# Performance work log

Hardware: AMD Instinct MI355X
Metric: run time of the kernel (lower is better)

## Reference

```python
import jax, jax.numpy as jnp
import numpy as np

N = 10000      # nodes
E = 320000     # edges
H = 128        # hidden_features
GF = 12        # graph-level features
L = 6          # gnn layers
EPS = 1e-5


def _glorot(key, shape):
    fan_in = shape[0]
    return (jax.random.normal(key, shape, jnp.float32) / np.sqrt(fan_in)).astype(jnp.float32)


def periodic_difference(x_i, x_j, domain):
    diff = x_i - x_j
    # (1 - 2*(x_i < x_j)) * domain  ==  +domain if x_i >= x_j else -domain
    shift = jnp.where(x_i < x_j, -domain, domain)
    diff_shifted = diff - shift
    return jnp.where(jnp.abs(diff) < jnp.abs(diff_shifted), diff, diff_shifted)


def _mlp2_relu(x, W1, b1, W2, b2):
    # Linear -> ReLU -> Linear -> ReLU
    return jax.nn.relu(jax.nn.relu(x @ W1 + b1) @ W2 + b2)


def setup_inputs() -> dict:
    key = jax.random.key(0)
    ks = jax.random.split(key, 32)
    inp = {
        "v": jax.random.normal(ks[0], (N, 6), jnp.float32),
        "pos": jax.random.uniform(ks[1], (N, 3), jnp.float32),
        "r": jax.random.uniform(ks[2], (N, 1), jnp.float32),
        "domain": jnp.ones((3,), jnp.float32),
        "t": jax.random.uniform(ks[3], (1,), jnp.float32),
        "x_global": jax.random.normal(ks[4], (4,), jnp.float32),
        "domain_next": jnp.ones((3,), jnp.float32),
        "t_next": jax.random.uniform(ks[5], (1,), jnp.float32),
        "edge_index": jax.random.randint(ks[6], (2, E), 0, N, jnp.int32),
        "batch": jnp.zeros((N,), jnp.int32),
    }
    # embedding MLP: 19 -> H -> H
    inp["emb_W1"] = _glorot(ks[7], (19, H)); inp["emb_b1"] = jnp.zeros((H,), jnp.float32)
    inp["emb_W2"] = _glorot(ks[8], (H, H)); inp["emb_b2"] = jnp.zeros((H,), jnp.float32)
    # per-layer message net: 157 -> H -> H ; update net: 268 -> H -> H
    msg_in = H + GF + 3 + 2 * (6 + 1)   # 157
    upd_in = H + H + GF                 # 268
    inp["msg_W1"] = jnp.stack([_glorot(jax.random.fold_in(ks[9], i), (msg_in, H)) for i in range(L)])
    inp["msg_b1"] = jnp.zeros((L, H), jnp.float32)
    inp["msg_W2"] = jnp.stack([_glorot(jax.random.fold_in(ks[10], i), (H, H)) for i in range(L)])
    inp["msg_b2"] = jnp.zeros((L, H), jnp.float32)
    inp["upd_W1"] = jnp.stack([_glorot(jax.random.fold_in(ks[11], i), (upd_in, H)) for i in range(L)])
    inp["upd_b1"] = jnp.zeros((L, H), jnp.float32)
    inp["upd_W2"] = jnp.stack([_glorot(jax.random.fold_in(ks[12], i), (H, H)) for i in range(L)])
    inp["upd_b2"] = jnp.zeros((L, H), jnp.float32)
    # output MLP: H -> H -> 9 ; macro MLP: H -> H -> 3
    inp["out_W1"] = _glorot(ks[13], (H, H)); inp["out_b1"] = jnp.zeros((H,), jnp.float32)
    inp["out_W2"] = _glorot(ks[14], (H, 9)); inp["out_b2"] = jnp.zeros((9,), jnp.float32)
    inp["mac_W1"] = _glorot(ks[15], (H, H)); inp["mac_b1"] = jnp.zeros((H,), jnp.float32)
    inp["mac_W2"] = _glorot(ks[16], (H, 3)); inp["mac_b2"] = jnp.zeros((3,), jnp.float32)
    return inp


def reference(v, pos, r, domain, t, x_global, domain_next, t_next, edge_index, batch,
              emb_W1, emb_b1, emb_W2, emb_b2,
              msg_W1, msg_b1, msg_W2, msg_b2,
              upd_W1, upd_b1, upd_W2, upd_b2,
              out_W1, out_b1, out_W2, out_b2,
              mac_W1, mac_b1, mac_W2, mac_b2):
    n = v.shape[0]
    gf = jnp.concatenate([domain, t, x_global, domain_next, t_next])          # [12]
    gf_n = jnp.broadcast_to(gf, (n, GF))
    node_features = jnp.concatenate([pos, v], axis=1)                         # [N, 9]

    # embedding (positions excluded)
    h = _mlp2_relu(jnp.concatenate([r, v, gf_n], axis=1), emb_W1, emb_b1, emb_W2, emb_b2)

    src, dst = edge_index[0], edge_index[1]   # j = source, i = target (PyG default)
    gf_e = jnp.broadcast_to(gf, (src.shape[0], GF))
    counts = jax.ops.segment_sum(jnp.ones(src.shape, h.dtype), dst, num_segments=N)
    inv_counts = (1.0 / jnp.maximum(counts, 1.0))[:, None]

    pos_diff = periodic_difference(pos[dst], pos[src], domain)                # [E, 3]
    v_i, v_j, r_i, r_j = v[dst], v[src], r[dst], r[src]

    for l in range(L):
        h_i, h_j = h[dst], h[src]
        msg_in = jnp.concatenate([h_i - h_j, v_i, v_j, r_i, r_j, pos_diff, gf_e], axis=1)
        m = _mlp2_relu(msg_in, msg_W1[l], msg_b1[l], msg_W2[l], msg_b2[l])    # [E, H]
        agg = jax.ops.segment_sum(m, dst, num_segments=N) * inv_counts        # scatter-mean
        upd_in = jnp.concatenate([h, agg, gf_n], axis=1)
        u = _mlp2_relu(upd_in, upd_W1[l], upd_b1[l], upd_W2[l], upd_b2[l])
        h = u + h                                                              # residual (in==out)
        # InstanceNorm over each graph (single graph here), biased variance
        mu = h.mean(axis=0, keepdims=True)
        var = h.var(axis=0, keepdims=True)
        h = (h - mu) / jnp.sqrt(var + EPS)

    prediction = jax.nn.relu(h @ out_W1 + out_b1) @ out_W2 + out_b2 + node_features
    pred_x = jnp.remainder(prediction[:, :3], domain_next)
    pred_v = prediction[:, 3:]
    h_mean = h.mean(axis=0)                                                    # global mean pool, 1 graph
    pred_macro = jax.nn.relu(h_mean @ mac_W1 + mac_b1) @ mac_W2 + mac_b2
    return pred_x, pred_v, pred_macro
```

## Files before the change

kernel.cpp:

```cpp
#include <hip/hip_runtime.h>
#include <hip/hip_bf16.h>

#define NN 10000
#define NE 320000
#define HD 128
#define NL 6
#define EPSV 1e-5f

typedef _Float16 half8  __attribute__((ext_vector_type(8)));
typedef _Float16 half4v __attribute__((ext_vector_type(4)));
typedef float    f32x4  __attribute__((ext_vector_type(4)));

__device__ __forceinline__ float relu_(float x){ return fmaxf(x, 0.0f); }


__global__ void k_degree(const int* __restrict__ dst, int* __restrict__ counts){
  int e = blockIdx.x*256 + threadIdx.x;
  if (e < NE) atomicAdd(&counts[dst[e]], 1);
}

__global__ void k_scan(const int* __restrict__ counts, int* __restrict__ offs, float* __restrict__ invc){
  __shared__ int lds[1024];
  __shared__ int base_s;
  int tid = threadIdx.x;
  if (tid==0) base_s = 0;
  __syncthreads();
  for (int start=0; start<NN; start+=1024){
    int i = start+tid;
    int vv = (i<NN)? counts[i] : 0;
    lds[tid]=vv; __syncthreads();
    for (int off=1; off<1024; off<<=1){
      int t = (tid>=off)? lds[tid-off] : 0;
      __syncthreads();
      lds[tid] += t;
      __syncthreads();
    }
    int incl = lds[tid];
    if (i<NN){
      offs[i] = base_s + incl - vv;
      invc[i] = 1.0f / fmaxf((float)vv, 1.0f);
    }
    __syncthreads();
    if (tid==1023) base_s += lds[1023];
    __syncthreads();
  }
  if (tid==0) offs[NN] = base_s;
}

__global__ void k_place(const int* __restrict__ src, const int* __restrict__ dst,
                        const int* __restrict__ offs, int* __restrict__ cursor, int* __restrict__ csr){
  int e = blockIdx.x*256 + threadIdx.x;
  if (e < NE){
    int d = dst[e];
    int p = atomicAdd(&cursor[d], 1);
    csr[offs[d]+p] = src[e];
  }
}


__global__ void k_biasfold(const float* __restrict__ dom, const float* __restrict__ tt,
                           const float* __restrict__ xg, const float* __restrict__ domn,
                           const float* __restrict__ tn,
                           const float* __restrict__ embW1, const float* __restrict__ embB1,
                           const float* __restrict__ msgW1, const float* __restrict__ msgB1,
                           const float* __restrict__ updW1, const float* __restrict__ updB1,
                           float* __restrict__ b1eff, float* __restrict__ mu, float* __restrict__ rstd){
  float gf[12];
  gf[0]=dom[0]; gf[1]=dom[1]; gf[2]=dom[2]; gf[3]=tt[0];
  gf[4]=xg[0]; gf[5]=xg[1]; gf[6]=xg[2]; gf[7]=xg[3];
  gf[8]=domn[0]; gf[9]=domn[1]; gf[10]=domn[2]; gf[11]=tn[0];
  int b = blockIdx.x, t = threadIdx.x;
  if (b==0){
    float s = embB1[t];
    #pragma unroll
    for (int k=0;k<12;++k) s += gf[k]*embW1[(7+k)*HD + t];
    b1eff[t] = s;
  } else if (b<=6){
    int l=b-1;
    float s = msgB1[l*HD+t];
    #pragma unroll
    for (int k=0;k<12;++k) s += gf[k]*msgW1[((size_t)l*157 + 145+k)*HD + t];
    b1eff[(1+l)*HD + t] = s;
  } else if (b<=12){
    int l=b-7;
    float s = updB1[l*HD+t];
    #pragma unroll
    for (int k=0;k<12;++k) s += gf[k]*updW1[((size_t)l*268 + 256+k)*HD + t];
    b1eff[(7+l)*HD + t] = s;
  } else {
    mu[t] = 0.f;
    rstd[t] = 1.f;
  }
}


__global__ void k_embed(const float* __restrict__ r, const float* __restrict__ v,
                        const float* __restrict__ W1, const float* __restrict__ b1e,
                        const float* __restrict__ W2, const float* __restrict__ b2,
                        float* __restrict__ hb){
  __shared__ alignas(16) float a1s[4][HD];
  int tid=threadIdx.x, wid=tid>>6, lane=tid&63;
  int gw = blockIdx.x*4 + wid;
  int f0=lane, f1=lane+64;
  float* a1 = a1s[wid];
  float b1f0=b1e[f0], b1f1=b1e[f1], b2f0=b2[f0], b2f1=b2[f1];
  for (int n=gw*4; n<gw*4+4; ++n){
    float in7[7];
    in7[0]=r[n];
    #pragma unroll
    for (int k=0;k<6;++k) in7[1+k]=v[n*6+k];
    float z0=b1f0, z1=b1f1;
    #pragma unroll
    for (int k=0;k<7;++k){ z0 += in7[k]*W1[k*HD+f0]; z1 += in7[k]*W1[k*HD+f1]; }
    a1[f0]=relu_(z0); a1[f1]=relu_(z1);
    float h0=b2f0, h1=b2f1;
    for (int k=0;k<HD;++k){ float a=a1[k]; h0+=a*W2[k*HD+f0]; h1+=a*W2[k*HD+f1]; }
    hb[n*HD+f0]=relu_(h0); hb[n*HD+f1]=relu_(h1);
  }
}


__global__ __launch_bounds__(512,1) void k_hW(
    const float* __restrict__ hb, const float* __restrict__ mu, const float* __restrict__ rstd,
    const float* __restrict__ v, const float* __restrict__ r,
    const float* __restrict__ W, const float* __restrict__ b1e,
    float* __restrict__ P, float* __restrict__ Q){
  __shared__ alignas(16) _Float16 Xhi[16*136];
  __shared__ alignas(16) _Float16 Xlo[16*136];
  int tid = threadIdx.x;
  int n0 = blockIdx.x*16;
  if (tid < 256){
    int node = tid>>4, chunk = tid&15;
    int n = n0 + node;
    int f = chunk*8;
    half8 xh, xl;
    #pragma unroll
    for (int j=0;j<8;++j){
      float x = (hb[(size_t)n*HD + f+j] - mu[f+j]) * rstd[f+j];
      _Float16 h = (_Float16)x;
      xh[j] = h; xl[j] = (_Float16)(x - (float)h);
    }
    *(half8*)&Xhi[node*136 + f] = xh;
    *(half8*)&Xlo[node*136 + f] = xl;
  }
  int wid = tid>>6, lane = tid&63, g = lane>>4, c = lane&15;
  int col = 16*wid + c;
  half8 bh[4], bl[4];
  #pragma unroll
  for (int ks=0; ks<4; ++ks){
    half8 fh, fl;
    #pragma unroll
    for (int j=0;j<8;++j){
      float w = W[(size_t)(ks*32 + g*8 + j)*HD + col];
      _Float16 h = (_Float16)w;
      fh[j]=h; fl[j]=(_Float16)(w - (float)h);
    }
    bh[ks]=fh; bl[ks]=fl;
  }
  float wvi[6], wvj[6];
  #pragma unroll
  for (int x=0;x<6;++x){
    wvi[x]=W[(size_t)(128+x)*HD+col];
    wvj[x]=W[(size_t)(134+x)*HD+col];
  }
  float wri=W[(size_t)140*HD+col], wrj=W[(size_t)141*HD+col];
  float b1c=b1e[col];
  f32x4 zero4 = {0.f,0.f,0.f,0.f};
  __syncthreads();
  f32x4 d = zero4;
  #pragma unroll
  for (int ks=0; ks<4; ++ks){
    half8 ah = *(const half8*)&Xhi[c*136 + ks*32 + g*8];
    half8 al = *(const half8*)&Xlo[c*136 + ks*32 + g*8];
    d = __builtin_amdgcn_mfma_f32_16x16x32_f16(ah, bh[ks], d, 0,0,0);
    d = __builtin_amdgcn_mfma_f32_16x16x32_f16(al, bh[ks], d, 0,0,0);
    d = __builtin_amdgcn_mfma_f32_16x16x32_f16(ah, bl[ks], d, 0,0,0);
  }
  #pragma unroll
  for (int jj=0;jj<4;++jj){
    int n = n0 + g*4 + jj;
    float m = d[jj];
    float p = m + b1c, q = -m;
    #pragma unroll
    for (int x=0;x<6;++x){
      float vx = v[n*6+x];
      p += vx*wvi[x]; q += vx*wvj[x];
    }
    float rn = r[n];
    p += rn*wri; q += rn*wrj;
    P[(size_t)n*HD+col]=p;
    Q[(size_t)n*HD+col]=q;
  }
}


__global__ __launch_bounds__(256,2) void k_edge(
    const float* __restrict__ P, const float* __restrict__ Q,
    const float* __restrict__ pos, const float* __restrict__ dom,
    const int* __restrict__ offs, const int* __restrict__ csr,
    const float* __restrict__ Wpd, const float* __restrict__ W2, const float* __restrict__ b2,
    const float* __restrict__ invc, float* __restrict__ agg,
    float* __restrict__ zsum, float* __restrict__ zsumsq){
  __shared__ alignas(16) _Float16 w1pd[128*40];
  __shared__ alignas(16) _Float16 a1hi[16*136];
  __shared__ alignas(16) _Float16 a1lo[16*136];
  int tid = threadIdx.x;
  if (blockIdx.x==0 && tid<HD){ zsum[tid]=0.f; zsumsq[tid]=0.f; }
  if (tid < 128){
    int f = tid;
    #pragma unroll
    for (int k=0;k<32;++k) w1pd[f*40+k] = (_Float16)0.f;
    #pragma unroll
    for (int x=0;x<3;++x){
      float w = Wpd[x*HD + f];
      _Float16 h = (_Float16)w;
      w1pd[f*40 + x]     = h;
      w1pd[f*40 + 3 + x] = h;
      w1pd[f*40 + 6 + x] = (_Float16)(w - (float)h);
    }
  }
  int wid = tid>>6, lane = tid&63, g = lane>>4, c = lane&15;
  int t0 = 2*wid, t1 = 2*wid+1;
  half8 w2h[4][2], w2l[4][2];
  #pragma unroll
  for (int ks=0; ks<4; ++ks){
    #pragma unroll
    for (int tt=0; tt<2; ++tt){
      int col = 16*(2*wid+tt) + c;
      half8 fh, fl;
      #pragma unroll
      for (int j=0;j<8;++j){
        float w = W2[(ks*32 + g*8 + j)*HD + col];
        _Float16 h = (_Float16)w;
        fh[j] = h;
        fl[j] = (_Float16)(w - (float)h);
      }
      w2h[ks][tt] = fh;
      w2l[ks][tt] = fl;
    }
  }
  float b2v0 = b2[16*t0 + c], b2v1 = b2[16*t1 + c];
  float dm0=dom[0], dm1=dom[1], dm2=dom[2];
  f32x4 zero4 = {0.f,0.f,0.f,0.f};
  __syncthreads();
  int n0 = blockIdx.x*4;
  for (int n = n0; n < n0+4; ++n){
    f32x4 pv0 = *(const f32x4*)(P + (size_t)n*HD + 16*t0 + 4*g);
    f32x4 pv1 = *(const f32x4*)(P + (size_t)n*HD + 16*t1 + 4*g);
    float pn0=pos[n*3+0], pn1=pos[n*3+1], pn2=pos[n*3+2];
    float acc0=0.f, acc1=0.f;
    int ib=offs[n], ie=offs[n+1];
    for (int base=ib; base<ie; base+=16){
      int nb = ie - base; if (nb>16) nb = 16;
      int sA = csr[base + ((c<nb)? c : nb-1)];
      float q0=pos[sA*3+0], q1=pos[sA*3+1], q2=pos[sA*3+2];
      float pd0,pd1,pd2;
      { float diff,sh,ds;
        diff=pn0-q0; sh=(pn0<q0)?-dm0:dm0; ds=diff-sh; pd0=(fabsf(diff)<fabsf(ds))?diff:ds;
        diff=pn1-q1; sh=(pn1<q1)?-dm1:dm1; ds=diff-sh; pd1=(fabsf(diff)<fabsf(ds))?diff:ds;
        diff=pn2-q2; sh=(pn2<q2)?-dm2:dm2; ds=diff-sh; pd2=(fabsf(diff)<fabsf(ds))?diff:ds;
      }
      _Float16 p0h = (_Float16)pd0, p1h = (_Float16)pd1, p2h = (_Float16)pd2;
      _Float16 p0l = (_Float16)(pd0 - (float)p0h);
      _Float16 p1l = (_Float16)(pd1 - (float)p1h);
      _Float16 p2l = (_Float16)(pd2 - (float)p2h);
      half8 pdf;
      #pragma unroll
      for (int j=0;j<8;++j) pdf[j]=(_Float16)0.f;
      if (g==0){ pdf[0]=p0h; pdf[1]=p1h; pdf[2]=p2h; pdf[3]=p0l; pdf[4]=p1l; pdf[5]=p2l; pdf[6]=p0h; pdf[7]=p1h; }
      else if (g==1){ pdf[0]=p2h; }
      half8 w1f0 = *(const half8*)&w1pd[(16*t0 + c)*40 + g*8];
      half8 w1f1 = *(const half8*)&w1pd[(16*t1 + c)*40 + g*8];
      f32x4 d0 = __builtin_amdgcn_mfma_f32_16x16x32_f16(w1f0, pdf, zero4, 0,0,0);
      f32x4 d1 = __builtin_amdgcn_mfma_f32_16x16x32_f16(w1f1, pdf, zero4, 0,0,0);
      const float* Qs = Q + (size_t)sA*HD;
      f32x4 qv0 = *(const f32x4*)(Qs + 16*t0 + 4*g);
      f32x4 qv1 = *(const f32x4*)(Qs + 16*t1 + 4*g);
      half4v h0, l0, h1, l1;
      #pragma unroll
      for (int j=0;j<4;++j){
        float a = fmaxf(d0[j] + pv0[j] + qv0[j], 0.f);
        _Float16 hh = (_Float16)a;
        h0[j] = hh; l0[j] = (_Float16)(a - (float)hh);
        float b = fmaxf(d1[j] + pv1[j] + qv1[j], 0.f);
        _Float16 hb2 = (_Float16)b;
        h1[j] = hb2; l1[j] = (_Float16)(b - (float)hb2);
      }
      *(half4v*)&a1hi[c*136 + 16*t0 + 4*g] = h0;
      *(half4v*)&a1lo[c*136 + 16*t0 + 4*g] = l0;
      *(half4v*)&a1hi[c*136 + 16*t1 + 4*g] = h1;
      *(half4v*)&a1lo[c*136 + 16*t1 + 4*g] = l1;
      __syncthreads();
      f32x4 m0 = zero4, m1 = zero4;
      #pragma unroll
      for (int ks=0; ks<4; ++ks){
        half8 ah = *(const half8*)&a1hi[c*136 + ks*32 + g*8];
        half8 al = *(const half8*)&a1lo[c*136 + ks*32 + g*8];
        m0 = __builtin_amdgcn_mfma_f32_16x16x32_f16(ah, w2h[ks][0], m0, 0,0,0);
        m0 = __builtin_amdgcn_mfma_f32_16x16x32_f16(al, w2h[ks][0], m0, 0,0,0);
        m0 = __builtin_amdgcn_mfma_f32_16x16x32_f16(ah, w2l[ks][0], m0, 0,0,0);
        m1 = __builtin_amdgcn_mfma_f32_16x16x32_f16(ah, w2h[ks][1], m1, 0,0,0);
        m1 = __builtin_amdgcn_mfma_f32_16x16x32_f16(al, w2h[ks][1], m1, 0,0,0);
        m1 = __builtin_amdgcn_mfma_f32_16x16x32_f16(ah, w2l[ks][1], m1, 0,0,0);
      }
      if (nb == 16){
        acc0 += fmaxf(m0[0]+b2v0,0.f)+fmaxf(m0[1]+b2v0,0.f)+fmaxf(m0[2]+b2v0,0.f)+fmaxf(m0[3]+b2v0,0.f);
        acc1 += fmaxf(m1[0]+b2v1,0.f)+fmaxf(m1[1]+b2v1,0.f)+fmaxf(m1[2]+b2v1,0.f)+fmaxf(m1[3]+b2v1,0.f);
      } else {
        #pragma unroll
        for (int j=0;j<4;++j){
          if (4*g+j < nb){
            acc0 += fmaxf(m0[j]+b2v0, 0.f);
            acc1 += fmaxf(m1[j]+b2v1, 0.f);
          }
        }
      }
      __syncthreads();
    }
    acc0 += __shfl_xor(acc0, 16); acc0 += __shfl_xor(acc0, 32);
    acc1 += __shfl_xor(acc1, 16); acc1 += __shfl_xor(acc1, 32);
    if (g==0){
      float ic = invc[n];
      agg[n*HD + 16*t0 + c] = acc0*ic;
      agg[n*HD + 16*t1 + c] = acc1*ic;
    }
  }
}


__global__ __launch_bounds__(512,1) void k_upd(
    float* __restrict__ hb, const float* __restrict__ mu, const float* __restrict__ rstd,
    const float* __restrict__ agg,
    const float* __restrict__ U1, const float* __restrict__ b1e,
    const float* __restrict__ U2, const float* __restrict__ bs2,
    float* __restrict__ sum, float* __restrict__ sumsq){
  __shared__ alignas(16) _Float16 Xhi[16*264];
  __shared__ alignas(16) _Float16 Xlo[16*264];
  __shared__ alignas(16) _Float16 Ahi[16*136];
  __shared__ alignas(16) _Float16 Alo[16*136];
  int tid = threadIdx.x;
  int n0 = blockIdx.x*16;
  {
    int node = tid>>5, chunk = tid&31;
    int n = n0 + node;
    int f = chunk*8;
    half8 xh, xl;
    if (f < 128){
      #pragma unroll
      for (int j=0;j<8;++j){
        float x = (hb[(size_t)n*HD + f+j] - mu[f+j]) * rstd[f+j];
        _Float16 h = (_Float16)x;
        xh[j] = h; xl[j] = (_Float16)(x - (float)h);
      }
    } else {
      #pragma unroll
      for (int j=0;j<8;++j){
        float x = agg[(size_t)n*HD + (f-128)+j];
        _Float16 h = (_Float16)x;
        xh[j] = h; xl[j] = (_Float16)(x - (float)h);
      }
    }
    *(half8*)&Xhi[node*264 + f] = xh;
    *(half8*)&Xlo[node*264 + f] = xl;
  }
  int wid = tid>>6, lane = tid&63, g = lane>>4, c = lane&15;
  int col = 16*wid + c;
  half8 b1h[8], b1l[8], b2h[4], b2l[4];
  #pragma unroll
  for (int ks=0; ks<8; ++ks){
    half8 fh, fl;
    #pragma unroll
    for (int j=0;j<8;++j){
      float w = U1[(size_t)(ks*32 + g*8 + j)*HD + col];
      _Float16 h = (_Float16)w;
      fh[j]=h; fl[j]=(_Float16)(w - (float)h);
    }
    b1h[ks]=fh; b1l[ks]=fl;
  }
  #pragma unroll
  for (int ks=0; ks<4; ++ks){
    half8 fh, fl;
    #pragma unroll
    for (int j=0;j<8;++j){
      float w = U2[(size_t)(ks*32 + g*8 + j)*HD + col];
      _Float16 h = (_Float16)w;
      fh[j]=h; fl[j]=(_Float16)(w - (float)h);
    }
    b2h[ks]=fh; b2l[ks]=fl;
  }
  f32x4 zero4 = {0.f,0.f,0.f,0.f};
  __syncthreads();
  f32x4 d = zero4;
  #pragma unroll
  for (int ks=0; ks<8; ++ks){
    half8 ah = *(const half8*)&Xhi[c*264 + ks*32 + g*8];
    half8 al = *(const half8*)&Xlo[c*264 + ks*32 + g*8];
    d = __builtin_amdgcn_mfma_f32_16x16x32_f16(ah, b1h[ks], d, 0,0,0);
    d = __builtin_amdgcn_mfma_f32_16x16x32_f16(al, b1h[ks], d, 0,0,0);
    d = __builtin_amdgcn_mfma_f32_16x16x32_f16(ah, b1l[ks], d, 0,0,0);
  }
  {
    float bb = b1e[col];
    #pragma unroll
    for (int jj=0;jj<4;++jj){
      float a = fmaxf(d[jj] + bb, 0.f);
      _Float16 h = (_Float16)a;
      Ahi[(g*4+jj)*136 + col] = h;
      Alo[(g*4+jj)*136 + col] = (_Float16)(a - (float)h);
    }
  }
  __syncthreads();
  f32x4 u = zero4;
  #pragma unroll
  for (int ks=0; ks<4; ++ks){
    half8 ah = *(const half8*)&Ahi[c*136 + ks*32 + g*8];
    half8 al = *(const half8*)&Alo[c*136 + ks*32 + g*8];
    u = __builtin_amdgcn_mfma_f32_16x16x32_f16(ah, b2h[ks], u, 0,0,0);
    u = __builtin_amdgcn_mfma_f32_16x16x32_f16(al, b2h[ks], u, 0,0,0);
    u = __builtin_amdgcn_mfma_f32_16x16x32_f16(ah, b2l[ks], u, 0,0,0);
  }
  float bc = bs2[col];
  float mc = mu[col], rc = rstd[col];
  float s=0.f, q=0.f;
  #pragma unroll
  for (int jj=0;jj<4;++jj){
    int n = n0 + g*4 + jj;
    float hn = (hb[(size_t)n*HD + col] - mc)*rc;
    float b0 = hn + fmaxf(u[jj] + bc, 0.f);
    hb[(size_t)n*HD + col] = b0;
    s += b0; q += b0*b0;
  }
  s += __shfl_xor(s,16); s += __shfl_xor(s,32);
  q += __shfl_xor(q,16); q += __shfl_xor(q,32);
  if (g==0){
    atomicAdd(&sum[col], s);
    atomicAdd(&sumsq[col], q);
  }
}

__global__ void k_normfin(const float* __restrict__ sum, const float* __restrict__ sumsq,
                          float* __restrict__ mu, float* __restrict__ rstd){
  int t=threadIdx.x;
  float m = sum[t]*(1.0f/NN);
  float var = sumsq[t]*(1.0f/NN) - m*m;
  mu[t]=m;
  rstd[t]=rsqrtf(fmaxf(var,0.0f)+EPSV);
}


__global__ void k_out(const float* __restrict__ hb, const float* __restrict__ mu, const float* __restrict__ rstd,
                      const float* __restrict__ pos, const float* __restrict__ v,
                      const float* __restrict__ W1, const float* __restrict__ b1,
                      const float* __restrict__ W2, const float* __restrict__ b2,
                      const float* __restrict__ domn, float* __restrict__ out){
  __shared__ alignas(16) float hs[4][HD*4];
  __shared__ alignas(16) float a1s[4][HD*4];
  int tid=threadIdx.x, wid=tid>>6, lane=tid&63;
  int gw=blockIdx.x*4+wid;
  int f0=lane, f1=lane+64;
  float* h4=hs[wid];
  float* a1p=a1s[wid];
  int n0=gw*4;
  float mu0=mu[f0], mu1=mu[f1], rs0=rstd[f0], rs1=rstd[f1];
  float4 hv0,hv1;
  hv0.x=(hb[(n0+0)*HD+f0]-mu0)*rs0; hv0.y=(hb[(n0+1)*HD+f0]-mu0)*rs0;
  hv0.z=(hb[(n0+2)*HD+f0]-mu0)*rs0; hv0.w=(hb[(n0+3)*HD+f0]-mu0)*rs0;
  hv1.x=(hb[(n0+0)*HD+f1]-mu1)*rs1; hv1.y=(hb[(n0+1)*HD+f1]-mu1)*rs1;
  hv1.z=(hb[(n0+2)*HD+f1]-mu1)*rs1; hv1.w=(hb[(n0+3)*HD+f1]-mu1)*rs1;
  *(float4*)&h4[f0*4]=hv0; *(float4*)&h4[f1*4]=hv1;
  float b1f0=b1[f0], b1f1=b1[f1];
  float zf0[4]={b1f0,b1f0,b1f0,b1f0}, zf1[4]={b1f1,b1f1,b1f1,b1f1};
  for (int k=0;k<HD;++k){
    float4 a = *(const float4*)&h4[k*4];
    float w0=W1[k*HD+f0], w1=W1[k*HD+f1];
    zf0[0]+=a.x*w0; zf1[0]+=a.x*w1;
    zf0[1]+=a.y*w0; zf1[1]+=a.y*w1;
    zf0[2]+=a.z*w0; zf1[2]+=a.z*w1;
    zf0[3]+=a.w*w0; zf1[3]+=a.w*w1;
  }
  *(float4*)&a1p[f0*4] = make_float4(relu_(zf0[0]),relu_(zf0[1]),relu_(zf0[2]),relu_(zf0[3]));
  *(float4*)&a1p[f1*4] = make_float4(relu_(zf1[0]),relu_(zf1[1]),relu_(zf1[2]),relu_(zf1[3]));
  if (lane < 36){
    int e = lane/9, j = lane - e*9;
    int n = n0+e;
    float p = b2[j];
    for (int k=0;k<HD;++k) p += a1p[k*4+e]*W2[k*9+j];
    if (j<3){
      p += pos[n*3+j];
      float d = domn[j];
      p = p - floorf(p/d)*d;
      out[n*3+j] = p;
    } else {
      p += v[n*6 + (j-3)];
      out[3*NN + n*6 + (j-3)] = p;
    }
  }
}

__global__ void k_macro(const float* __restrict__ sum, const float* __restrict__ mu, const float* __restrict__ rstd,
                        const float* __restrict__ W1, const float* __restrict__ b1,
                        const float* __restrict__ W2, const float* __restrict__ b2,
                        float* __restrict__ out){
  __shared__ float hm[HD];
  __shared__ float as[HD];
  int t=threadIdx.x;
  hm[t] = (sum[t]*(1.0f/NN) - mu[t])*rstd[t];
  __syncthreads();
  float z=b1[t];
  for (int k=0;k<HD;++k) z += hm[k]*W1[k*HD+t];
  as[t]=relu_(z);
  __syncthreads();
  if (t<3){
    float p=b2[t];
    for (int k=0;k<HD;++k) p += as[k]*W2[k*3+t];
    out[9*NN+t]=p;
  }
}


extern "C" void kernel_launch(void* const* d_in, const int* in_sizes, int n_in,
                              void* d_out, int out_size, void* d_ws, size_t ws_size,
                              hipStream_t stream) {
  const float* v    = (const float*)d_in[0];
  const float* pos  = (const float*)d_in[1];
  const float* r    = (const float*)d_in[2];
  const float* dom  = (const float*)d_in[3];
  const float* tt   = (const float*)d_in[4];
  const float* xg   = (const float*)d_in[5];
  const float* domn = (const float*)d_in[6];
  const float* tn   = (const float*)d_in[7];
  const int*   eidx = (const int*)d_in[8];
  const float* embW1 = (const float*)d_in[10];
  const float* embB1 = (const float*)d_in[11];
  const float* embW2 = (const float*)d_in[12];
  const float* embB2 = (const float*)d_in[13];
  const float* msgW1 = (const float*)d_in[14];
  const float* msgB1 = (const float*)d_in[15];
  const float* msgW2 = (const float*)d_in[16];
  const float* msgB2 = (const float*)d_in[17];
  const float* updW1 = (const float*)d_in[18];
  const float* updB1 = (const float*)d_in[19];
  const float* updW2 = (const float*)d_in[20];
  const float* updB2 = (const float*)d_in[21];
  const float* outW1 = (const float*)d_in[22];
  const float* outB1 = (const float*)d_in[23];
  const float* outW2 = (const float*)d_in[24];
  const float* outB2 = (const float*)d_in[25];
  const float* macW1 = (const float*)d_in[26];
  const float* macB1 = (const float*)d_in[27];
  const float* macW2 = (const float*)d_in[28];
  const float* macB2 = (const float*)d_in[29];
  float* out = (float*)d_out;
  float* ws  = (float*)d_ws;

  float* hb    = ws;
  float* P     = ws + 1280000;
  float* Q     = ws + 2560000;
  float* agg   = ws + 3840000;
  float* invc  = ws + 5120000;
  float* b1eff = ws + 5130000;
  float* sum   = ws + 5131664;
  float* sumsq = ws + 5131792;
  float* mu    = ws + 5131920;
  float* rstd  = ws + 5132048;
  int* counts  = (int*)(ws + 5132304);
  int* offs    = counts + NN;
  int* cursor  = offs + NN + 1;
  int* csr     = cursor + NN;

  const int* srcA = eidx;
  const int* dstA = eidx + NE;

  hipMemsetAsync(counts, 0, NN*sizeof(int), stream);
  hipMemsetAsync(cursor, 0, NN*sizeof(int), stream);

  k_degree<<<(NE+255)/256, 256, 0, stream>>>(dstA, counts);
  k_scan<<<1, 1024, 0, stream>>>(counts, offs, invc);
  k_place<<<(NE+255)/256, 256, 0, stream>>>(srcA, dstA, offs, cursor, csr);
  k_biasfold<<<14, 128, 0, stream>>>(dom, tt, xg, domn, tn, embW1, embB1, msgW1, msgB1, updW1, updB1,
                                     b1eff, mu, rstd);
  k_embed<<<625, 256, 0, stream>>>(r, v, embW1, b1eff, embW2, embB2, hb);

  for (int l=0; l<NL; ++l){
    k_hW<<<625,512,0,stream>>>(hb, mu, rstd, v, r, msgW1 + (size_t)l*157*HD, b1eff + (1+l)*HD, P, Q);
    k_edge<<<2500,256,0,stream>>>(P, Q, pos, dom, offs, csr,
        msgW1 + ((size_t)l*157+142)*HD,
        msgW2 + (size_t)l*HD*HD, msgB2 + l*HD, invc, agg, sum, sumsq);
    k_upd<<<625,512,0,stream>>>(hb, mu, rstd, agg,
        updW1 + (size_t)l*268*HD, b1eff + (7+l)*HD,
        updW2 + (size_t)l*HD*HD, updB2 + l*HD, sum, sumsq);
    k_normfin<<<1,128,0,stream>>>(sum, sumsq, mu, rstd);
  }

  k_out<<<625,256,0,stream>>>(hb, mu, rstd, pos, v, outW1, outB1, outW2, outB2, domn, out);
  k_macro<<<1,128,0,stream>>>(sum, mu, rstd, macW1, macB1, macW2, macB2, out);
}
```

Baseline: 855.6 us.

## Move embedding MLP to split-fp16 MFMA and halve nodes per edge block

The embedding kernel's second layer now runs on 16x16x32 fp16 MFMA with hi/lo split operands, 16 nodes per 512-thread block, instead of scalar FMA loops. Separately, the per-layer edge kernel handles 2 destination nodes per block instead of 4, doubling the grid to 5000 blocks for better load balance and occupancy. This costs more per-block setup, since the W2 fragments are reloaded per block.

```diff
diff --git a/kernel.cpp b/kernel.cpp
--- a/kernel.cpp
+++ b/kernel.cpp
@@ -94,28 +94,66 @@
 }
 
 
-__global__ void k_embed(const float* __restrict__ r, const float* __restrict__ v,
-                        const float* __restrict__ W1, const float* __restrict__ b1e,
-                        const float* __restrict__ W2, const float* __restrict__ b2,
-                        float* __restrict__ hb){
-  __shared__ alignas(16) float a1s[4][HD];
-  int tid=threadIdx.x, wid=tid>>6, lane=tid&63;
-  int gw = blockIdx.x*4 + wid;
-  int f0=lane, f1=lane+64;
-  float* a1 = a1s[wid];
-  float b1f0=b1e[f0], b1f1=b1e[f1], b2f0=b2[f0], b2f1=b2[f1];
-  for (int n=gw*4; n<gw*4+4; ++n){
+__global__ __launch_bounds__(512,1) void k_embed(
+    const float* __restrict__ r, const float* __restrict__ v,
+    const float* __restrict__ W1, const float* __restrict__ b1e,
+    const float* __restrict__ W2, const float* __restrict__ b2,
+    float* __restrict__ hb){
+  __shared__ alignas(16) _Float16 Ahi[16*136];
+  __shared__ alignas(16) _Float16 Alo[16*136];
+  int tid = threadIdx.x;
+  int n0 = blockIdx.x*16;
+  if (tid < 256){
+    int node = tid>>4, chunk = tid&15;
+    int n = n0 + node;
+    int f = chunk*8;
     float in7[7];
     in7[0]=r[n];
     #pragma unroll
     for (int k=0;k<6;++k) in7[1+k]=v[n*6+k];
-    float z0=b1f0, z1=b1f1;
-    #pragma unroll
-    for (int k=0;k<7;++k){ z0 += in7[k]*W1[k*HD+f0]; z1 += in7[k]*W1[k*HD+f1]; }
-    a1[f0]=relu_(z0); a1[f1]=relu_(z1);
-    float h0=b2f0, h1=b2f1;
-    for (int k=0;k<HD;++k){ float a=a1[k]; h0+=a*W2[k*HD+f0]; h1+=a*W2[k*HD+f1]; }
-    hb[n*HD+f0]=relu_(h0); hb[n*HD+f1]=relu_(h1);
+    half8 ah, al;
+    #pragma unroll
+    for (int j=0;j<8;++j){
+      float z = b1e[f+j];
+      #pragma unroll
+      for (int k=0;k<7;++k) z += in7[k]*W1[k*HD + f+j];
+      float a = fmaxf(z, 0.f);
+      _Float16 h = (_Float16)a;
+      ah[j] = h; al[j] = (_Float16)(a - (float)h);
+    }
+    *(half8*)&Ahi[node*136 + f] = ah;
+    *(half8*)&Alo[node*136 + f] = al;
+  }
+  int wid = tid>>6, lane = tid&63, g = lane>>4, c = lane&15;
+  int col = 16*wid + c;
+  half8 bh[4], bl[4];
+  #pragma unroll
+  for (int ks=0; ks<4; ++ks){
+    half8 fh, fl;
+    #pragma unroll
+    for (int j=0;j<8;++j){
+      float w = W2[(size_t)(ks*32 + g*8 + j)*HD + col];
+      _Float16 h = (_Float16)w;
+      fh[j]=h; fl[j]=(_Float16)(w - (float)h);
+    }
+    bh[ks]=fh; bl[ks]=fl;
+  }
+  float b2c = b2[col];
+  f32x4 zero4 = {0.f,0.f,0.f,0.f};
+  __syncthreads();
+  f32x4 d = zero4;
+  #pragma unroll
+  for (int ks=0; ks<4; ++ks){
+    half8 ah = *(const half8*)&Ahi[c*136 + ks*32 + g*8];
+    half8 al = *(const half8*)&Alo[c*136 + ks*32 + g*8];
+    d = __builtin_amdgcn_mfma_f32_16x16x32_f16(ah, bh[ks], d, 0,0,0);
+    d = __builtin_amdgcn_mfma_f32_16x16x32_f16(al, bh[ks], d, 0,0,0);
+    d = __builtin_amdgcn_mfma_f32_16x16x32_f16(ah, bl[ks], d, 0,0,0);
+  }
+  #pragma unroll
+  for (int jj=0;jj<4;++jj){
+    int n = n0 + g*4 + jj;
+    hb[(size_t)n*HD + col] = fmaxf(d[jj] + b2c, 0.f);
   }
 }
 
@@ -243,8 +281,8 @@
   float dm0=dom[0], dm1=dom[1], dm2=dom[2];
   f32x4 zero4 = {0.f,0.f,0.f,0.f};
   __syncthreads();
-  int n0 = blockIdx.x*4;
-  for (int n = n0; n < n0+4; ++n){
+  int n0 = blockIdx.x*2;
+  for (int n = n0; n < n0+2; ++n){
     f32x4 pv0 = *(const f32x4*)(P + (size_t)n*HD + 16*t0 + 4*g);
     f32x4 pv1 = *(const f32x4*)(P + (size_t)n*HD + 16*t1 + 4*g);
     float pn0=pos[n*3+0], pn1=pos[n*3+1], pn2=pos[n*3+2];
@@ -579,11 +617,11 @@
   k_place<<<(NE+255)/256, 256, 0, stream>>>(srcA, dstA, offs, cursor, csr);
   k_biasfold<<<14, 128, 0, stream>>>(dom, tt, xg, domn, tn, embW1, embB1, msgW1, msgB1, updW1, updB1,
                                      b1eff, mu, rstd);
-  k_embed<<<625, 256, 0, stream>>>(r, v, embW1, b1eff, embW2, embB2, hb);
+  k_embed<<<625, 512, 0, stream>>>(r, v, embW1, b1eff, embW2, embB2, hb);
 
   for (int l=0; l<NL; ++l){
     k_hW<<<625,512,0,stream>>>(hb, mu, rstd, v, r, msgW1 + (size_t)l*157*HD, b1eff + (1+l)*HD, P, Q);
-    k_edge<<<2500,256,0,stream>>>(P, Q, pos, dom, offs, csr,
+    k_edge<<<5000,256,0,stream>>>(P, Q, pos, dom, offs, csr,
         msgW1 + ((size_t)l*157+142)*HD,
         msgW2 + (size_t)l*HD*HD, msgB2 + l*HD, invc, agg, sum, sumsq);
     k_upd<<<625,512,0,stream>>>(hb, mu, rstd, agg,
```

New measurement: 840.7 us. No clear change (-1.7%).
